# Performance work log

Measured on AMD Instinct MI355X. Metric: run time of the kernel, lower is better.

The kernel has to match this reference:

```python
import jax, jax.numpy as jnp
import numpy as np

B, S, DM, H = 2, 2048, 1024, 16
HD = DM // H
SCALE = 1.0 / np.sqrt(HD)  # temperature = 1.0
LN_EPS = 1e-5


def setup_inputs() -> dict:
    key = jax.random.key(0)
    ks = jax.random.split(key, 12)
    s = 1.0 / np.sqrt(DM)
    inp = {
        'x': jax.random.normal(ks[0], (B, S, DM), dtype=jnp.float32),
        'Wq': jax.random.uniform(ks[1], (DM, DM), jnp.float32, -s, s),
        'bq': jnp.zeros((DM,), jnp.float32),
        'Wk': jax.random.uniform(ks[2], (DM, DM), jnp.float32, -s, s),
        'bk': jnp.zeros((DM,), jnp.float32),
        'Wv': jax.random.uniform(ks[3], (DM, DM), jnp.float32, -s, s),
        'bv': jnp.zeros((DM,), jnp.float32),
        'Wo': jax.random.uniform(ks[4], (DM, DM), jnp.float32, -s, s),
        'bo': jnp.zeros((DM,), jnp.float32),
        'Wg': jax.random.uniform(ks[5], (DM, DM), jnp.float32, -s, s),
        'bg': jnp.zeros((DM,), jnp.float32),
        'attention_weights': jnp.ones((H,), jnp.float32),
        'ln_gamma': jnp.ones((DM,), jnp.float32),
        'ln_beta': jnp.zeros((DM,), jnp.float32),
    }
    return inp


def _forward(x, Wq, bq, Wk, bk, Wv, bv, Wo, bo, Wg, bg, attention_weights, ln_gamma, ln_beta):
    # projections -> [B, H, S, HD]
    def split_heads(t):
        return t.reshape(B, S, H, HD).transpose(0, 2, 1, 3)
    q = split_heads(x @ Wq.T + bq)
    k = split_heads(x @ Wk.T + bk)
    v = split_heads(x @ Wv.T + bv)
    # scores [B, H, S, S]; no softmax: exact-erf GELU activation instead
    scores = jnp.einsum('bhsd,bhtd->bhst', q, k) * SCALE
    attn = jax.nn.gelu(scores, approximate=False)
    head_w = jax.nn.softmax(attention_weights)  # [H]
    attn = attn * head_w[None, :, None, None]
    # context [B, S, DM]
    ctx = jnp.einsum('bhst,bhtd->bhsd', attn, v).transpose(0, 2, 1, 3).reshape(B, S, DM)
    out = ctx @ Wo.T + bo
    gate = jax.nn.sigmoid(out @ Wg.T + bg)
    out = gate * out + (1.0 - gate) * x
    y = out + x
    mu = jnp.mean(y, axis=-1, keepdims=True)
    var = jnp.var(y, axis=-1, keepdims=True)
    return (y - mu) / jnp.sqrt(var + LN_EPS) * ln_gamma + ln_beta


def reference(x, Wq, bq, Wk, bk, Wv, bv, Wo, bo, Wg, bg, attention_weights, ln_gamma, ln_beta):
    return _forward(x, Wq, bq, Wk, bk, Wv, bv, Wo, bo, Wg, bg, attention_weights, ln_gamma, ln_beta)
```

## Files before the change

kernel.cpp:

```cpp
#include <hip/hip_runtime.h>
#include <hip/hip_bf16.h>

#define B_ 2
#define S_ 2048
#define DM_ 1024
#define H_ 16
#define HD_ 64
#define QKVLD 3072
#define WELT_ ((size_t)DM_ * DM_)

using bf16x8 = __attribute__((ext_vector_type(8))) short;
using f32x4  = __attribute__((ext_vector_type(4))) float;
using f32x16 = __attribute__((ext_vector_type(16))) float;

#define GLOAD16(g, l) __builtin_amdgcn_global_load_lds( \
    (const __attribute__((address_space(1))) void*)(g), \
    (__attribute__((address_space(3))) void*)(l), 16, 0, 0)

__device__ __forceinline__ int swz128(int row, int bytecol) {
    return row * 128 + (bytecol ^ ((row & 7) << 4));
}

__device__ __forceinline__ float gelu_poly(float x) {
    float u = x * x;
    float t = fmaf(-0.00074855f, u, 0.0146724f);
    t = fmaf(t, u, -0.1266945f);
    t = fmaf(t, u, 0.7966101f);
    float e = x * t;
    e = fminf(fmaxf(e, -1.0f), 1.0f);
    float hx = 0.5f * x;
    return fmaf(hx, e, hx);
}

__device__ __forceinline__ ushort bf16_rne(float f) {
    uint b = __builtin_bit_cast(uint, f);
    b += 0x7FFF + ((b >> 16) & 1);
    return (ushort)(b >> 16);
}

__device__ __forceinline__ float bf16_to_f(ushort u) {
    return __builtin_bit_cast(float, (uint)u << 16);
}

__device__ __forceinline__ uint cvtpk(float lo, float hi) {
    uint r;
    asm("v_cvt_pk_bf16_f32 %0, %1, %2" : "=v"(r) : "v"(lo), "v"(hi));
    return r;
}
__device__ __forceinline__ void pl32swap(uint& a, uint& b) {
    asm volatile("v_permlane32_swap_b32 %0, %1" : "+v"(a), "+v"(b));
}

__global__ __launch_bounds__(256) void cast_bf16_kernel(const float* __restrict__ in,
                                                        __hip_bfloat16* __restrict__ out, int n) {
    int i = (blockIdx.x * 256 + threadIdx.x) * 4;
    if (i >= n) return;
    float4 v = *(const float4*)(in + i);
    ushort4 o = { bf16_rne(v.x), bf16_rne(v.y), bf16_rne(v.z), bf16_rne(v.w) };
    *(ushort4*)(out + i) = o;
}

__global__ __launch_bounds__(256) void prep_kernel(
    const float* __restrict__ Wq, const float* __restrict__ Wk, const float* __restrict__ Wv,
    const float* __restrict__ Wo, const float* __restrict__ Wg,
    const float* __restrict__ bq, const float* __restrict__ bk, const float* __restrict__ bv,
    const float* __restrict__ aw, __hip_bfloat16* __restrict__ Wdst, float* __restrict__ bqkv)
{
    auto headw = [&](int h) {
        float mx = aw[0];
        for (int i = 1; i < H_; ++i) mx = fmaxf(mx, aw[i]);
        float sm = 0.f;
        for (int i = 0; i < H_; ++i) sm += expf(aw[i] - mx);
        return expf(aw[h] - mx) / sm;
    };
    int blk = blockIdx.x;
    if (blk < 5120) {
        int widx = blk >> 10;
        int row = blk & 1023;
        int off = row * 1024 + threadIdx.x * 4;
        const float* src = widx == 0 ? Wq : widx == 1 ? Wk : widx == 2 ? Wv : widx == 3 ? Wo : Wg;
        float scale = widx == 0 ? 0.125f : 1.0f;
        if (widx == 2) scale = headw(row >> 6);
        float4 v = *(const float4*)(src + off);
        ushort4 o = { bf16_rne(v.x * scale), bf16_rne(v.y * scale),
                      bf16_rne(v.z * scale), bf16_rne(v.w * scale) };
        *(ushort4*)(Wdst + widx * WELT_ + off) = o;
    } else {
        int i = (blk - 5120) * 256 + threadIdx.x;
        if (i < 3 * DM_) {
            float v;
            if (i < DM_) v = bq[i] * 0.125f;
            else if (i < 2 * DM_) v = bk[i - DM_];
            else v = bv[i - 2 * DM_] * headw((i - 2 * DM_) >> 6);
            bqkv[i] = v;
        }
    }
}

__global__ __launch_bounds__(256, 2) void gemm_nt_kernel(
    const __hip_bfloat16* __restrict__ A, int lda,
    const __hip_bfloat16* __restrict__ Bw, int ldb,
    const float* __restrict__ bias, float* __restrict__ Cf,
    __hip_bfloat16* __restrict__ Cb, int ldc, int M, int N, int K)
{
    __shared__ __align__(16) char smem[32768];
    const int tid = threadIdx.x;
    const int w = tid >> 6, lane = tid & 63, hi = lane >> 4, lo = lane & 15;
    const int wr = w >> 1, wc = w & 1;
    const int m0 = blockIdx.y * 128, n0 = blockIdx.x * 128;

    const int srow = lane >> 3;
    const int scol = (lane & 7) ^ srow;
    const __hip_bfloat16* sbase;
    int sld;
    char* lbase;
    if (w < 2) {
        sbase = A + (size_t)(m0 + w * 64 + srow) * lda + scol * 8;
        sld = lda;
        lbase = smem + w * 8192;
    } else {
        sbase = Bw + (size_t)(n0 + (w - 2) * 64 + srow) * ldb + scol * 8;
        sld = ldb;
        lbase = smem + 16384 + (w - 2) * 8192;
    }

    f32x4 acc[4][4];
#pragma unroll
    for (int m = 0; m < 4; ++m)
#pragma unroll
        for (int n = 0; n < 4; ++n) acc[m][n] = (f32x4){0.f, 0.f, 0.f, 0.f};

    for (int k0 = 0; k0 < K; k0 += 64) {
#pragma unroll
        for (int i = 0; i < 8; ++i)
            GLOAD16(sbase + (size_t)i * 8 * sld + k0, lbase + i * 1024);
        __syncthreads();
#pragma unroll
        for (int ks = 0; ks < 2; ++ks) {
            bf16x8 af[4], bfr[4];
#pragma unroll
            for (int m = 0; m < 4; ++m)
                af[m] = *(const bf16x8*)(smem + swz128(wr * 64 + m * 16 + lo, ks * 64 + hi * 16));
#pragma unroll
            for (int n = 0; n < 4; ++n)
                bfr[n] = *(const bf16x8*)(smem + 16384 + swz128(wc * 64 + n * 16 + lo, ks * 64 + hi * 16));
#pragma unroll
            for (int m = 0; m < 4; ++m)
#pragma unroll
                for (int n = 0; n < 4; ++n)
                    acc[m][n] = __builtin_amdgcn_mfma_f32_16x16x32_bf16(af[m], bfr[n], acc[m][n], 0, 0, 0);
        }
        __syncthreads();
    }

#pragma unroll
    for (int n = 0; n < 4; ++n) {
        int gc = n0 + wc * 64 + n * 16 + lo;
        float bz = bias[gc];
#pragma unroll
        for (int m = 0; m < 4; ++m) {
            int gr = m0 + wr * 64 + m * 16 + hi * 4;
#pragma unroll
            for (int r = 0; r < 4; ++r) {
                float v = acc[m][n][r] + bz;
                size_t o = (size_t)(gr + r) * ldc + gc;
                if (Cf) Cf[o] = v;
                if (Cb) *(ushort*)(Cb + o) = bf16_rne(v);
            }
        }
    }
}

__global__ __launch_bounds__(256) void transpose_v_kernel(const __hip_bfloat16* __restrict__ QKV,
                                                          __hip_bfloat16* __restrict__ Vt) {
    __shared__ __align__(16) ushort tile[64][80];
    const int tid = threadIdx.x;
    const int nt = S_ / 64;
    const int blk = blockIdx.x;
    const int t0 = (blk % nt) * 64;
    const int bh = blk / nt;
    const int h = bh % H_, b = bh / H_;
#pragma unroll
    for (int c = tid; c < 512; c += 256) {
        int row = c >> 3, cg = c & 7;
        float4 v = *(const float4*)(QKV + (size_t)(b * S_ + t0 + row) * QKVLD + 2 * DM_ + h * HD_ + cg * 8);
        *(float4*)(&tile[row][cg * 8]) = v;
    }
    __syncthreads();
#pragma unroll
    for (int c = tid; c < 512; c += 256) {
        int d = c >> 3, tg = c & 7;
        union { ushort u[8]; float4 v; } tmp;
#pragma unroll
        for (int j = 0; j < 8; ++j) tmp.u[j] = tile[tg * 8 + j][d];
        *(float4*)(Vt + ((size_t)(b * H_ + h) * HD_ + d) * S_ + t0 + tg * 8) = tmp.v;
    }
}

__global__ __launch_bounds__(256) void attn_kernel(
    const __hip_bfloat16* __restrict__ QKV, const __hip_bfloat16* __restrict__ Vt,
    __hip_bfloat16* __restrict__ ctx)
{
    __shared__ __align__(16) char lds[2][16384];

    const int tid = threadIdx.x;
    const int w = tid >> 6, lane = tid & 63;
    const int l31 = lane & 31, hi2 = lane >> 5;
    const int nq = S_ / 128;
    int blk = blockIdx.x;
    blk = (blk & 7) * 64 + (blk >> 3);
    const int q0 = (blk % nq) * 128;
    const int bh = blk / nq;
    const int h = bh % H_, b = bh / H_;

    bf16x8 qf[4];
    {
        const __hip_bfloat16* qrow = QKV + ((size_t)(b * S_ + q0 + w * 32 + l31) * QKVLD + h * HD_);
#pragma unroll
        for (int ks = 0; ks < 4; ++ks)
            qf[ks] = *(const bf16x8*)(qrow + ks * 16 + hi2 * 8);
    }

    const bool isK = (w < 2);
    const int fb = (w & 1) * 4;
    const __hip_bfloat16* sp[4];
    int ldsoff[4];
#pragma unroll
    for (int j = 0; j < 4; ++j) {
        int f = fb + j;
        if (isK) {
            sp[j] = QKV + (size_t)(b * S_ + (f >> 2) * 32 + l31) * QKVLD + DM_ + h * HD_ + (f & 3) * 16 + hi2 * 8;
            ldsoff[j] = f * 1024;
        } else {
            sp[j] = Vt + ((size_t)((b * H_ + h) * HD_) + (f >> 2) * 32 + l31) * S_ + (f & 3) * 16 + hi2 * 8;
            ldsoff[j] = 8192 + f * 1024;
        }
    }
    const size_t tstep = isK ? (size_t)64 * QKVLD : (size_t)64;

#define STAGE(buf) do { \
    _Pragma("unroll") \
    for (int j = 0; j < 4; ++j) { \
        GLOAD16(sp[j], lds[buf] + ldsoff[j]); \
        sp[j] += tstep; \
    } } while (0)

    f32x16 cacc[2];
#pragma unroll
    for (int n = 0; n < 2; ++n)
#pragma unroll
        for (int r = 0; r < 16; ++r) cacc[n][r] = 0.f;

    STAGE(0);
    asm volatile("s_waitcnt vmcnt(0)" ::: "memory");
    __builtin_amdgcn_s_barrier();

    const int lane16 = lane * 16;
    for (int t = 0; t < S_ / 64; ++t) {
        const int cur = t & 1;
        if (t + 1 < S_ / 64) STAGE(cur ^ 1);

#pragma unroll
        for (int n = 0; n < 2; ++n) {
            f32x16 sacc;
#pragma unroll
            for (int r = 0; r < 16; ++r) sacc[r] = 0.f;
#pragma unroll
            for (int ks = 0; ks < 4; ++ks) {
                bf16x8 kf = *(const bf16x8*)(lds[cur] + (n * 4 + ks) * 1024 + lane16);
                sacc = __builtin_amdgcn_mfma_f32_32x32x16_bf16(kf, qf[ks], sacc, 0, 0, 0);
            }
            float p[16];
#pragma unroll
            for (int r = 0; r < 16; ++r) p[r] = gelu_poly(sacc[r]);
            uint a0 = cvtpk(p[0], p[1]),   b0 = cvtpk(p[4], p[5]);
            uint a1 = cvtpk(p[2], p[3]),   b1 = cvtpk(p[6], p[7]);
            uint a2 = cvtpk(p[8], p[9]),   b2 = cvtpk(p[12], p[13]);
            uint a3 = cvtpk(p[10], p[11]), b3 = cvtpk(p[14], p[15]);
            pl32swap(a0, b0); pl32swap(a1, b1); pl32swap(a2, b2); pl32swap(a3, b3);
            union { uint u[4]; bf16x8 v; } pa0, pa1;
            pa0.u[0] = a0; pa0.u[1] = a1; pa0.u[2] = b0; pa0.u[3] = b1;
            pa1.u[0] = a2; pa1.u[1] = a3; pa1.u[2] = b2; pa1.u[3] = b3;
#pragma unroll
            for (int kc2 = 0; kc2 < 2; ++kc2) {
                int kc = n * 2 + kc2;
                bf16x8 pa = kc2 ? pa1.v : pa0.v;
#pragma unroll
                for (int n2 = 0; n2 < 2; ++n2) {
                    bf16x8 vf = *(const bf16x8*)(lds[cur] + 8192 + (n2 * 4 + kc) * 1024 + lane16);
                    cacc[n2] = __builtin_amdgcn_mfma_f32_32x32x16_bf16(pa, vf, cacc[n2], 0, 0, 0);
                }
            }
        }
        asm volatile("s_waitcnt vmcnt(0)" ::: "memory");
        __builtin_amdgcn_s_barrier();
    }

#pragma unroll
    for (int n2 = 0; n2 < 2; ++n2)
#pragma unroll
        for (int r = 0; r < 16; ++r) {
            int qrow = (r & 3) + 8 * (r >> 2) + 4 * hi2;
            size_t o = (size_t)(b * S_ + q0 + w * 32 + qrow) * DM_ + h * HD_ + n2 * 32 + l31;
            *(ushort*)(ctx + o) = bf16_rne(cacc[n2][r]);
        }
#undef STAGE
}

__global__ __launch_bounds__(256) void epilogue_ln_kernel(
    const __hip_bfloat16* __restrict__ outb, const __hip_bfloat16* __restrict__ gpreb,
    const float* __restrict__ x, const float* __restrict__ gamma,
    const float* __restrict__ beta, float* __restrict__ y)
{
    const int row = blockIdx.x, tid = threadIdx.x;
    const size_t base = (size_t)row * DM_ + tid * 4;
    ushort4 ob = *(const ushort4*)(outb + base);
    ushort4 gb = *(const ushort4*)(gpreb + base);
    float4 xv = *(const float4*)(x + base);
    float yv[4];
    float s = 0.f, s2 = 0.f;
    const ushort* obp = (const ushort*)&ob;
    const ushort* gbp = (const ushort*)&gb;
#pragma unroll
    for (int j = 0; j < 4; ++j) {
        float o = bf16_to_f(obp[j]), g = bf16_to_f(gbp[j]), xx = ((float*)&xv)[j];
        float gate = __builtin_amdgcn_rcpf(1.f + __expf(-g));
        float yy = gate * o + (1.f - gate) * xx + xx;
        yv[j] = yy;
        s += yy; s2 += yy * yy;
    }
    const int w = tid >> 6, lane = tid & 63;
#pragma unroll
    for (int off = 32; off > 0; off >>= 1) {
        s  += __shfl_down(s, off, 64);
        s2 += __shfl_down(s2, off, 64);
    }
    __shared__ float red[8];
    if (lane == 0) { red[w] = s; red[4 + w] = s2; }
    __syncthreads();
    s  = red[0] + red[1] + red[2] + red[3];
    s2 = red[4] + red[5] + red[6] + red[7];
    const float mu = s * (1.f / DM_);
    const float var = s2 * (1.f / DM_) - mu * mu;
    const float rstd = rsqrtf(var + 1e-5f);
    float4 outv;
#pragma unroll
    for (int j = 0; j < 4; ++j) {
        int col = tid * 4 + j;
        ((float*)&outv)[j] = (yv[j] - mu) * rstd * gamma[col] + beta[col];
    }
    *(float4*)(y + base) = outv;
}

extern "C" void kernel_launch(void* const* d_in, const int* in_sizes, int n_in,
                              void* d_out, int out_size, void* d_ws, size_t ws_size,
                              hipStream_t stream) {
    const float* x  = (const float*)d_in[0];
    const float* Wq = (const float*)d_in[1];
    const float* bq = (const float*)d_in[2];
    const float* Wk = (const float*)d_in[3];
    const float* bk = (const float*)d_in[4];
    const float* Wv = (const float*)d_in[5];
    const float* bv = (const float*)d_in[6];
    const float* Wo = (const float*)d_in[7];
    const float* bo = (const float*)d_in[8];
    const float* Wg = (const float*)d_in[9];
    const float* bg = (const float*)d_in[10];
    const float* aw = (const float*)d_in[11];
    const float* gamma = (const float*)d_in[12];
    const float* beta  = (const float*)d_in[13];

    char* ws = (char*)d_ws;
    size_t off = 0;
    auto alloc = [&](size_t bytes) -> char* {
        char* p = ws + off;
        off += (bytes + 255) & ~(size_t)255;
        return p;
    };
    const size_t NTOK = (size_t)B_ * S_;
    const size_t NELT = NTOK * DM_;

    __hip_bfloat16* xb    = (__hip_bfloat16*)alloc(NELT * 2);
    __hip_bfloat16* Wall  = (__hip_bfloat16*)alloc(5 * WELT_ * 2);
    float*          bqkv  = (float*)alloc(3 * DM_ * 4);
    __hip_bfloat16* qkvb  = (__hip_bfloat16*)alloc(NTOK * QKVLD * 2);
    __hip_bfloat16* Vtb   = (__hip_bfloat16*)alloc(NELT * 2);
    __hip_bfloat16* ctxb  = (__hip_bfloat16*)alloc(NELT * 2);
    __hip_bfloat16* outb  = (__hip_bfloat16*)alloc(NELT * 2);
    __hip_bfloat16* gpreb = (__hip_bfloat16*)alloc(NELT * 2);

    cast_bf16_kernel<<<(int)(NELT / 1024), 256, 0, stream>>>(x, xb, (int)NELT);
    prep_kernel<<<5120 + 12, 256, 0, stream>>>(Wq, Wk, Wv, Wo, Wg, bq, bk, bv, aw, Wall, bqkv);

    gemm_nt_kernel<<<dim3(QKVLD / 128, (int)(NTOK / 128)), 256, 0, stream>>>(
        xb, DM_, Wall, DM_, bqkv, nullptr, qkvb, QKVLD, (int)NTOK, QKVLD, DM_);

    transpose_v_kernel<<<B_ * H_ * (S_ / 64), 256, 0, stream>>>(qkvb, Vtb);
    attn_kernel<<<B_ * H_ * (S_ / 128), 256, 0, stream>>>(qkvb, Vtb, ctxb);

    gemm_nt_kernel<<<dim3(DM_ / 128, (int)(NTOK / 128)), 256, 0, stream>>>(
        ctxb, DM_, Wall + 3 * WELT_, DM_, bo, nullptr, outb, DM_, (int)NTOK, DM_, DM_);
    gemm_nt_kernel<<<dim3(DM_ / 128, (int)(NTOK / 128)), 256, 0, stream>>>(
        outb, DM_, Wall + 4 * WELT_, DM_, bg, nullptr, gpreb, DM_, (int)NTOK, DM_, DM_);

    epilogue_ln_kernel<<<(int)NTOK, 256, 0, stream>>>(outb, gpreb, x, gamma, beta, (float*)d_out);
}
```

Baseline: 162.1 us.

## Split attention KV tiles across warp pairs and fuse x cast into prep kernel

The attention kernel now handles 64 query rows per block instead of 128. Two warps share each 32-row query group, and each warp processes half of every 64-key tile. Their partial context accumulators are summed through LDS at the end. This doubles the grid and sets launch bounds to 4 blocks per SM to raise occupancy, at the cost of loading K/V tiles twice as often overall plus a final reduction. Separately, the x-to-bf16 cast is merged into the weight prep kernel to drop one launch.

```diff
diff --git a/kernel.cpp b/kernel.cpp
--- a/kernel.cpp
+++ b/kernel.cpp
@@ -51,16 +51,8 @@
     asm volatile("v_permlane32_swap_b32 %0, %1" : "+v"(a), "+v"(b));
 }
 
-__global__ __launch_bounds__(256) void cast_bf16_kernel(const float* __restrict__ in,
-                                                        __hip_bfloat16* __restrict__ out, int n) {
-    int i = (blockIdx.x * 256 + threadIdx.x) * 4;
-    if (i >= n) return;
-    float4 v = *(const float4*)(in + i);
-    ushort4 o = { bf16_rne(v.x), bf16_rne(v.y), bf16_rne(v.z), bf16_rne(v.w) };
-    *(ushort4*)(out + i) = o;
-}
-
 __global__ __launch_bounds__(256) void prep_kernel(
+    const float* __restrict__ x, __hip_bfloat16* __restrict__ xb,
     const float* __restrict__ Wq, const float* __restrict__ Wk, const float* __restrict__ Wv,
     const float* __restrict__ Wo, const float* __restrict__ Wg,
     const float* __restrict__ bq, const float* __restrict__ bk, const float* __restrict__ bv,
@@ -74,7 +66,13 @@
         return expf(aw[h] - mx) / sm;
     };
     int blk = blockIdx.x;
-    if (blk < 5120) {
+    if (blk < 4096) {
+        int i = blk * 1024 + threadIdx.x * 4;
+        float4 v = *(const float4*)(x + i);
+        ushort4 o = { bf16_rne(v.x), bf16_rne(v.y), bf16_rne(v.z), bf16_rne(v.w) };
+        *(ushort4*)(xb + i) = o;
+    } else if (blk < 9216) {
+        blk -= 4096;
         int widx = blk >> 10;
         int row = blk & 1023;
         int off = row * 1024 + threadIdx.x * 4;
@@ -86,7 +84,7 @@
                       bf16_rne(v.z * scale), bf16_rne(v.w * scale) };
         *(ushort4*)(Wdst + widx * WELT_ + off) = o;
     } else {
-        int i = (blk - 5120) * 256 + threadIdx.x;
+        int i = (blk - 9216) * 256 + threadIdx.x;
         if (i < 3 * DM_) {
             float v;
             if (i < DM_) v = bq[i] * 0.125f;
@@ -197,7 +195,7 @@
     }
 }
 
-__global__ __launch_bounds__(256) void attn_kernel(
+__global__ __launch_bounds__(256, 4) void attn_kernel(
     const __hip_bfloat16* __restrict__ QKV, const __hip_bfloat16* __restrict__ Vt,
     __hip_bfloat16* __restrict__ ctx)
 {
@@ -206,16 +204,17 @@
     const int tid = threadIdx.x;
     const int w = tid >> 6, lane = tid & 63;
     const int l31 = lane & 31, hi2 = lane >> 5;
-    const int nq = S_ / 128;
+    const int qg = w & 1, th = w >> 1;
+    const int nq = S_ / 64;
     int blk = blockIdx.x;
-    blk = (blk & 7) * 64 + (blk >> 3);
-    const int q0 = (blk % nq) * 128;
+    blk = (blk & 7) * 128 + (blk >> 3);
+    const int q0 = (blk % nq) * 64;
     const int bh = blk / nq;
     const int h = bh % H_, b = bh / H_;
 
     bf16x8 qf[4];
     {
-        const __hip_bfloat16* qrow = QKV + ((size_t)(b * S_ + q0 + w * 32 + l31) * QKVLD + h * HD_);
+        const __hip_bfloat16* qrow = QKV + ((size_t)(b * S_ + q0 + qg * 32 + l31) * QKVLD + h * HD_);
 #pragma unroll
         for (int ks = 0; ks < 4; ++ks)
             qf[ks] = *(const bf16x8*)(qrow + ks * 16 + hi2 * 8);
@@ -260,50 +259,60 @@
         const int cur = t & 1;
         if (t + 1 < S_ / 64) STAGE(cur ^ 1);
 
-#pragma unroll
-        for (int n = 0; n < 2; ++n) {
-            f32x16 sacc;
-#pragma unroll
-            for (int r = 0; r < 16; ++r) sacc[r] = 0.f;
-#pragma unroll
-            for (int ks = 0; ks < 4; ++ks) {
-                bf16x8 kf = *(const bf16x8*)(lds[cur] + (n * 4 + ks) * 1024 + lane16);
-                sacc = __builtin_amdgcn_mfma_f32_32x32x16_bf16(kf, qf[ks], sacc, 0, 0, 0);
-            }
-            float p[16];
-#pragma unroll
-            for (int r = 0; r < 16; ++r) p[r] = gelu_poly(sacc[r]);
-            uint a0 = cvtpk(p[0], p[1]),   b0 = cvtpk(p[4], p[5]);
-            uint a1 = cvtpk(p[2], p[3]),   b1 = cvtpk(p[6], p[7]);
-            uint a2 = cvtpk(p[8], p[9]),   b2 = cvtpk(p[12], p[13]);
-            uint a3 = cvtpk(p[10], p[11]), b3 = cvtpk(p[14], p[15]);
-            pl32swap(a0, b0); pl32swap(a1, b1); pl32swap(a2, b2); pl32swap(a3, b3);
-            union { uint u[4]; bf16x8 v; } pa0, pa1;
-            pa0.u[0] = a0; pa0.u[1] = a1; pa0.u[2] = b0; pa0.u[3] = b1;
-            pa1.u[0] = a2; pa1.u[1] = a3; pa1.u[2] = b2; pa1.u[3] = b3;
-#pragma unroll
-            for (int kc2 = 0; kc2 < 2; ++kc2) {
-                int kc = n * 2 + kc2;
-                bf16x8 pa = kc2 ? pa1.v : pa0.v;
-#pragma unroll
-                for (int n2 = 0; n2 < 2; ++n2) {
-                    bf16x8 vf = *(const bf16x8*)(lds[cur] + 8192 + (n2 * 4 + kc) * 1024 + lane16);
-                    cacc[n2] = __builtin_amdgcn_mfma_f32_32x32x16_bf16(pa, vf, cacc[n2], 0, 0, 0);
-                }
+        f32x16 sacc;
+#pragma unroll
+        for (int r = 0; r < 16; ++r) sacc[r] = 0.f;
+#pragma unroll
+        for (int ks = 0; ks < 4; ++ks) {
+            bf16x8 kf = *(const bf16x8*)(lds[cur] + (th * 4 + ks) * 1024 + lane16);
+            sacc = __builtin_amdgcn_mfma_f32_32x32x16_bf16(kf, qf[ks], sacc, 0, 0, 0);
+        }
+        float p[16];
+#pragma unroll
+        for (int r = 0; r < 16; ++r) p[r] = gelu_poly(sacc[r]);
+        uint a0 = cvtpk(p[0], p[1]),   b0 = cvtpk(p[4], p[5]);
+        uint a1 = cvtpk(p[2], p[3]),   b1 = cvtpk(p[6], p[7]);
+        uint a2 = cvtpk(p[8], p[9]),   b2 = cvtpk(p[12], p[13]);
+        uint a3 = cvtpk(p[10], p[11]), b3 = cvtpk(p[14], p[15]);
+        pl32swap(a0, b0); pl32swap(a1, b1); pl32swap(a2, b2); pl32swap(a3, b3);
+        union { uint u[4]; bf16x8 v; } pa0, pa1;
+        pa0.u[0] = a0; pa0.u[1] = a1; pa0.u[2] = b0; pa0.u[3] = b1;
+        pa1.u[0] = a2; pa1.u[1] = a3; pa1.u[2] = b2; pa1.u[3] = b3;
+#pragma unroll
+        for (int kc2 = 0; kc2 < 2; ++kc2) {
+            int kc = th * 2 + kc2;
+            bf16x8 pa = kc2 ? pa1.v : pa0.v;
+#pragma unroll
+            for (int n2 = 0; n2 < 2; ++n2) {
+                bf16x8 vf = *(const bf16x8*)(lds[cur] + 8192 + (n2 * 4 + kc) * 1024 + lane16);
+                cacc[n2] = __builtin_amdgcn_mfma_f32_32x32x16_bf16(pa, vf, cacc[n2], 0, 0, 0);
             }
         }
         asm volatile("s_waitcnt vmcnt(0)" ::: "memory");
         __builtin_amdgcn_s_barrier();
     }
 
-#pragma unroll
-    for (int n2 = 0; n2 < 2; ++n2)
-#pragma unroll
-        for (int r = 0; r < 16; ++r) {
-            int qrow = (r & 3) + 8 * (r >> 2) + 4 * hi2;
-            size_t o = (size_t)(b * S_ + q0 + w * 32 + qrow) * DM_ + h * HD_ + n2 * 32 + l31;
-            *(ushort*)(ctx + o) = bf16_rne(cacc[n2][r]);
-        }
+    char* red = lds[0];
+    if (th == 1) {
+#pragma unroll
+        for (int n2 = 0; n2 < 2; ++n2)
+#pragma unroll
+            for (int r = 0; r < 16; ++r)
+                *(float*)(red + qg * 8192 + (n2 * 16 + r) * 256 + lane * 4) = cacc[n2][r];
+    }
+    __syncthreads();
+    if (th == 0) {
+#pragma unroll
+        for (int n2 = 0; n2 < 2; ++n2)
+#pragma unroll
+            for (int r = 0; r < 16; ++r) {
+                float v = cacc[n2][r] +
+                    *(const float*)(red + qg * 8192 + (n2 * 16 + r) * 256 + lane * 4);
+                int qrow = (r & 3) + 8 * (r >> 2) + 4 * hi2;
+                size_t o = (size_t)(b * S_ + q0 + qg * 32 + qrow) * DM_ + h * HD_ + n2 * 32 + l31;
+                *(ushort*)(ctx + o) = bf16_rne(v);
+            }
+    }
 #undef STAGE
 }
 
@@ -389,14 +398,14 @@
     __hip_bfloat16* outb  = (__hip_bfloat16*)alloc(NELT * 2);
     __hip_bfloat16* gpreb = (__hip_bfloat16*)alloc(NELT * 2);
 
-    cast_bf16_kernel<<<(int)(NELT / 1024), 256, 0, stream>>>(x, xb, (int)NELT);
-    prep_kernel<<<5120 + 12, 256, 0, stream>>>(Wq, Wk, Wv, Wo, Wg, bq, bk, bv, aw, Wall, bqkv);
+    prep_kernel<<<9216 + 12, 256, 0, stream>>>(x, xb, Wq, Wk, Wv, Wo, Wg,
+                                               bq, bk, bv, aw, Wall, bqkv);
 
     gemm_nt_kernel<<<dim3(QKVLD / 128, (int)(NTOK / 128)), 256, 0, stream>>>(
         xb, DM_, Wall, DM_, bqkv, nullptr, qkvb, QKVLD, (int)NTOK, QKVLD, DM_);
 
     transpose_v_kernel<<<B_ * H_ * (S_ / 64), 256, 0, stream>>>(qkvb, Vtb);
-    attn_kernel<<<B_ * H_ * (S_ / 128), 256, 0, stream>>>(qkvb, Vtb, ctxb);
+    attn_kernel<<<B_ * H_ * (S_ / 64), 256, 0, stream>>>(qkvb, Vtb, ctxb);
 
     gemm_nt_kernel<<<dim3(DM_ / 128, (int)(NTOK / 128)), 256, 0, stream>>>(
         ctxb, DM_, Wall + 3 * WELT_, DM_, bo, nullptr, outb, DM_, (int)NTOK, DM_, DM_);
```

Result: slower. 167.3 us (+3.3%).
